# Optimization experiments

Hardware: AMD Instinct MI355X
Metric: run time of the kernel (lower is better)

## Reference

```python
import jax, jax.numpy as jnp
import numpy as np
from jax import lax

DN = ('NCDHW', 'OIDHW', 'NCDHW')


def conv3(x, w, stride=1):
    return lax.conv_general_dilated(x, w, (stride,) * 3, 'VALID', dimension_numbers=DN)


def edge_pad(v):  # zero-gradient (Neumann) halo of width 1
    return jnp.pad(v, ((0, 0), (0, 0), (1, 1), (1, 1), (1, 1)), mode='edge')


def zero_pad(v):  # Dirichlet-0 halo for the MG correction
    return jnp.pad(v, ((0, 0), (0, 0), (1, 1), (1, 1), (1, 1)))


def bc_u(u, ub):  # Neumann everywhere, Dirichlet inlet (u=ub) on -x face
    p = edge_pad(u)
    return p.at[:, :, :, :, 0].set(jnp.asarray(ub, p.dtype))


def prol(x):  # nearest-neighbour upsample x2 (nn.Upsample scale_factor=2)
    for ax in (2, 3, 4):
        x = jnp.repeat(x, 2, axis=ax)
    return x


def setup_inputs() -> dict:
    N = 128
    key = jax.random.key(0)
    k = jax.random.split(key, 6)
    shp = (1, 1, N, N, N)
    # 7-point Laplacian stencil (A and diff)
    wA = np.zeros((1, 1, 3, 3, 3), np.float32)
    wA[0, 0, 1, 1, 1] = -6.0
    for d, h, w in [(0, 1, 1), (2, 1, 1), (1, 0, 1), (1, 2, 1), (1, 1, 0), (1, 1, 2)]:
        wA[0, 0, d, h, w] = 1.0
    w_diff = wA.copy()
    # central-difference advection stencils along W (x), H (y), D (z)
    w_xadv = np.zeros((1, 1, 3, 3, 3), np.float32)
    w_xadv[0, 0, 1, 1, 0], w_xadv[0, 0, 1, 1, 2] = -0.5, 0.5
    w_yadv = np.zeros((1, 1, 3, 3, 3), np.float32)
    w_yadv[0, 0, 1, 0, 1], w_yadv[0, 0, 1, 2, 1] = -0.5, 0.5
    w_zadv = np.zeros((1, 1, 3, 3, 3), np.float32)
    w_zadv[0, 0, 0, 1, 1], w_zadv[0, 0, 2, 1, 1] = -0.5, 0.5
    w_res = np.full((1, 1, 2, 2, 2), 0.125, np.float32)
    return {
        'values_u': jax.random.normal(k[0], shp, jnp.float32) * 0.1,
        'values_v': jax.random.normal(k[1], shp, jnp.float32) * 0.1,
        'values_w': jax.random.normal(k[2], shp, jnp.float32) * 0.1,
        'values_p': jax.random.normal(k[3], shp, jnp.float32) * 0.1,
        'sigma': jax.random.uniform(k[4], shp, jnp.float32) * 10.0,  # solid-body drag field
        'dt': jnp.asarray(0.05, jnp.float32),
        'wA': jnp.asarray(wA), 'w_diff': jnp.asarray(w_diff),
        'w_xadv': jnp.asarray(w_xadv), 'w_yadv': jnp.asarray(w_yadv),
        'w_zadv': jnp.asarray(w_zadv), 'w_res': jnp.asarray(w_res),
        'ub': 1, 'Re': 1, 'iteration': 2, 'nlevel': 9,
    }


def reference(values_u, values_v, values_w, values_p, sigma, dt,
              wA, w_diff, w_xadv, w_yadv, w_zadv, w_res,
              ub, Re, iteration, nlevel):
    diag = wA[0, 0, 1, 1, 1]
    A = lambda x: conv3(x, wA)
    diff = lambda x: conv3(x, w_diff)
    xadv = lambda x: conv3(x, w_xadv)
    yadv = lambda x: conv3(x, w_yadv)
    zadv = lambda x: conv3(x, w_zadv)
    res = lambda x: conv3(x, w_res, stride=2)

    def solid(u, v, w):
        f = 1.0 / (1.0 + dt * sigma)
        return u * f, v * f, w * f

    def pg(uu, vv, ww, u, v, w):  # Petrov-Galerkin dissipation (k fields == 1)
        one = jnp.ones_like(u)
        kp = edge_pad(one)
        ku = 0.5 * (one * diff(uu) + diff(uu * kp) - u * diff(kp))
        kv = 0.5 * (one * diff(vv) + diff(vv * kp) - v * diff(kp))
        kw = 0.5 * (one * diff(ww) + diff(ww * kp) - w * diff(kp))
        return ku, kv, kw

    u, v, w = solid(values_u, values_v, values_w)
    uu, vv, ww = bc_u(u, ub), edge_pad(v), edge_pad(w)
    pp = edge_pad(values_p)
    ku, kv, kw = pg(uu, vv, ww, u, v, w)
    # half-step predictor
    b_u = u + 0.5 * (Re * ku * dt - u * xadv(uu) * dt - v * yadv(uu) * dt - w * zadv(uu) * dt) - xadv(pp) * dt
    b_v = v + 0.5 * (Re * kv * dt - u * xadv(vv) * dt - v * yadv(vv) * dt - w * zadv(vv) * dt) - yadv(pp) * dt
    b_w = w + 0.5 * (Re * kw * dt - u * xadv(ww) * dt - v * yadv(ww) * dt - w * zadv(ww) * dt) - zadv(pp) * dt
    b_u, b_v, b_w = solid(b_u, b_v, b_w)
    buu, bvv, bww = bc_u(b_u, ub), edge_pad(b_v), edge_pad(b_w)
    ku, kv, kw = pg(buu, bvv, bww, b_u, b_v, b_w)
    # full-step corrector
    u = u + Re * ku * dt - b_u * xadv(buu) * dt - b_v * yadv(buu) * dt - b_w * zadv(buu) * dt - xadv(pp) * dt
    v = v + Re * kv * dt - b_u * xadv(bvv) * dt - b_v * yadv(bvv) * dt - b_w * zadv(bvv) * dt - yadv(pp) * dt
    w = w + Re * kw * dt - b_u * xadv(bww) * dt - b_v * yadv(bww) * dt - b_w * zadv(bww) * dt - zadv(pp) * dt
    u, v, w = solid(u, v, w)
    uu, vv, ww = bc_u(u, ub), edge_pad(v), edge_pad(w)
    # multigrid F-cycle pressure solve
    b = -(xadv(uu) + yadv(vv) + zadv(ww)) / dt
    p = values_p
    wmg = jnp.zeros((1, 1, 1, 1, 1), u.dtype)
    r = b
    for _ in range(iteration):
        wmg = jnp.zeros((1, 1, 1, 1, 1), u.dtype)
        r = A(pp) - b
        r_s = [r]
        for _i in range(1, nlevel - 1):
            r = res(r)
            r_s.append(r)
        for i in reversed(range(1, nlevel - 1)):
            wp = zero_pad(wmg)
            wmg = wmg - A(wp) / diag + r_s[i] / diag
            wmg = prol(wmg)
        p = p - wmg
        p = p - A(pp) / diag + b / diag
        pp = edge_pad(p)
    u = u - xadv(pp) * dt
    v = v - yadv(pp) * dt
    w = w - zadv(pp) * dt
    u, v, w = solid(u, v, w)
    return u, v, w, p, wmg, r
```

## Files before the change

### kernel.cpp

```cpp
#include <hip/hip_runtime.h>

#define NN 128
#define VV (NN*NN*NN)

typedef float v4 __attribute__((ext_vector_type(4)));

__device__ __forceinline__ float rcpf(float a){ return __builtin_amdgcn_rcpf(a); }
__device__ __forceinline__ v4 rcp4(v4 a){ v4 r; r.x=rcpf(a.x); r.y=rcpf(a.y); r.z=rcpf(a.z); r.w=rcpf(a.w); return r; }
__device__ __forceinline__ v4 LD4(const float* __restrict__ F, int o){ return *(const v4*)(F+o); }
__device__ __forceinline__ v4 mk4(float a,float b,float c,float d){ v4 r; r.x=a;r.y=b;r.z=c;r.w=d; return r; }

__device__ __forceinline__ int clampi(int a, int lo, int hi){ return min(max(a,lo),hi); }
__device__ __forceinline__ float ldc(const float* __restrict__ f, int z, int y, int x){
    z=clampi(z,0,NN-1); y=clampi(y,0,NN-1); x=clampi(x,0,NN-1);
    return f[(z*NN+y)*NN+x];
}

#define SETUP_OFFS \
    int i4 = (blockIdx.x*blockDim.x + threadIdx.x)<<2; \
    int x = i4 & 127, y = (i4>>7)&127, z = i4>>14; \
    bool x0 = (x==0), x1 = (x==124); \
    int o_c  = i4; \
    int o_ym = o_c + ((y>0)   ? -128   : 0); \
    int o_yp = o_c + ((y<127) ?  128   : 0); \
    int o_zm = o_c + ((z>0)   ? -16384 : 0); \
    int o_zp = o_c + ((z<127) ?  16384 : 0); \
    int o_xm = x0 ? o_c : o_c-1; \
    int o_xp = x1 ? o_c : o_c+4;

__global__ void __launch_bounds__(256) k_predict(
        const float* __restrict__ u_in, const float* __restrict__ v_in,
        const float* __restrict__ w_in, const float* __restrict__ p,
        const float* __restrict__ sg, const float* __restrict__ dtp,
        const int* __restrict__ ubp, const int* __restrict__ rep,
        float* __restrict__ bu, float* __restrict__ bv, float* __restrict__ bw){
    SETUP_OFFS
    float dt = dtp[0], ub = (float)ubp[0], Re = (float)rep[0];
    float h = 0.5f*dt;

    v4 f_c  = rcp4(1.0f + dt*LD4(sg,o_c));
    v4 f_ym = rcp4(1.0f + dt*LD4(sg,o_ym));
    v4 f_yp = rcp4(1.0f + dt*LD4(sg,o_yp));
    v4 f_zm = rcp4(1.0f + dt*LD4(sg,o_zm));
    v4 f_zp = rcp4(1.0f + dt*LD4(sg,o_zp));
    float f_xm = rcpf(1.0f + dt*sg[o_xm]);
    float f_xp = rcpf(1.0f + dt*sg[o_xp]);

#define STEN(F, cen, vxm, vxp, vym, vyp, vzm, vzp, XMVAL) \
    v4 cen = LD4(F,o_c)*f_c; \
    v4 vym = LD4(F,o_ym)*f_ym; v4 vyp = LD4(F,o_yp)*f_yp; \
    v4 vzm = LD4(F,o_zm)*f_zm; v4 vzp = LD4(F,o_zp)*f_zp; \
    float cen##_xms = x0 ? (XMVAL) : F[o_xm]*f_xm; \
    float cen##_xps = x1 ? cen.w   : F[o_xp]*f_xp; \
    v4 vxm = mk4(cen##_xms, cen.x, cen.y, cen.z); \
    v4 vxp = mk4(cen.y, cen.z, cen.w, cen##_xps);

    STEN(u_in, uc, uxm, uxp, uym, uyp, uzm, uzp, ub)
    STEN(v_in, vc, vxm, vxp, vym, vyp, vzm, vzp, vc.x)
    STEN(w_in, wc, wxm, wxp, wym, wyp, wzm, wzp, wc.x)
#undef STEN

    v4 pc = LD4(p,o_c);
    v4 pym = LD4(p,o_ym), pyp = LD4(p,o_yp), pzm = LD4(p,o_zm), pzp = LD4(p,o_zp);
    float p_xms = x0 ? pc.x : p[o_xm];
    float p_xps = x1 ? pc.w : p[o_xp];
    v4 pxm = mk4(p_xms, pc.x, pc.y, pc.z);
    v4 pxp = mk4(pc.y, pc.z, pc.w, p_xps);
    v4 gpx = 0.5f*(pxp-pxm), gpy = 0.5f*(pyp-pym), gpz = 0.5f*(pzp-pzm);

    v4 lap_u = uxm+uxp+uym+uyp+uzm+uzp - 6.0f*uc;
    v4 lap_v = vxm+vxp+vym+vyp+vzm+vzp - 6.0f*vc;
    v4 lap_w = wxm+wxp+wym+wyp+wzm+wzp - 6.0f*wc;
    v4 xau=0.5f*(uxp-uxm), yau=0.5f*(uyp-uym), zau=0.5f*(uzp-uzm);
    v4 xav=0.5f*(vxp-vxm), yav=0.5f*(vyp-vym), zav=0.5f*(vzp-vzm);
    v4 xaw=0.5f*(wxp-wxm), yaw=0.5f*(wyp-wym), zaw=0.5f*(wzp-wzm);

    *(v4*)(bu+o_c) = (uc + h*(Re*lap_u - (uc*xau + vc*yau + wc*zau)) - dt*gpx)*f_c;
    *(v4*)(bv+o_c) = (vc + h*(Re*lap_v - (uc*xav + vc*yav + wc*zav)) - dt*gpy)*f_c;
    *(v4*)(bw+o_c) = (wc + h*(Re*lap_w - (uc*xaw + vc*yaw + wc*zaw)) - dt*gpz)*f_c;
}

__global__ void __launch_bounds__(256) k_corr(
        const float* __restrict__ u_in, const float* __restrict__ v_in,
        const float* __restrict__ w_in,
        const float* __restrict__ bu, const float* __restrict__ bv,
        const float* __restrict__ bw, const float* __restrict__ p,
        const float* __restrict__ sg, const float* __restrict__ dtp,
        const int* __restrict__ ubp, const int* __restrict__ rep,
        float* __restrict__ ou, float* __restrict__ ov, float* __restrict__ ow){
    SETUP_OFFS
    float dt = dtp[0], ub = (float)ubp[0], Re = (float)rep[0];
    v4 f0 = rcp4(1.0f + dt*LD4(sg,o_c));
    v4 u0c = LD4(u_in,o_c)*f0, v0c = LD4(v_in,o_c)*f0, w0c = LD4(w_in,o_c)*f0;

#define STEN2(F, cen, vxm, vxp, vym, vyp, vzm, vzp, XMVAL) \
    v4 cen = LD4(F,o_c); \
    v4 vym = LD4(F,o_ym), vyp = LD4(F,o_yp), vzm = LD4(F,o_zm), vzp = LD4(F,o_zp); \
    float cen##_xms = x0 ? (XMVAL) : F[o_xm]; \
    float cen##_xps = x1 ? cen.w   : F[o_xp]; \
    v4 vxm = mk4(cen##_xms, cen.x, cen.y, cen.z); \
    v4 vxp = mk4(cen.y, cen.z, cen.w, cen##_xps);

    STEN2(bu, uc, uxm, uxp, uym, uyp, uzm, uzp, ub)
    STEN2(bv, vc, vxm, vxp, vym, vyp, vzm, vzp, vc.x)
    STEN2(bw, wc, wxm, wxp, wym, wyp, wzm, wzp, wc.x)

    v4 pc = LD4(p,o_c);
    v4 pym = LD4(p,o_ym), pyp = LD4(p,o_yp), pzm = LD4(p,o_zm), pzp = LD4(p,o_zp);
    float p_xms = x0 ? pc.x : p[o_xm];
    float p_xps = x1 ? pc.w : p[o_xp];
    v4 pxm = mk4(p_xms, pc.x, pc.y, pc.z);
    v4 pxp = mk4(pc.y, pc.z, pc.w, p_xps);
    v4 gpx = 0.5f*(pxp-pxm), gpy = 0.5f*(pyp-pym), gpz = 0.5f*(pzp-pzm);

    v4 lap_u = uxm+uxp+uym+uyp+uzm+uzp - 6.0f*uc;
    v4 lap_v = vxm+vxp+vym+vyp+vzm+vzp - 6.0f*vc;
    v4 lap_w = wxm+wxp+wym+wyp+wzm+wzp - 6.0f*wc;
    v4 xau=0.5f*(uxp-uxm), yau=0.5f*(uyp-uym), zau=0.5f*(uzp-uzm);
    v4 xav=0.5f*(vxp-vxm), yav=0.5f*(vyp-vym), zav=0.5f*(vzp-vzm);
    v4 xaw=0.5f*(wxp-wxm), yaw=0.5f*(wyp-wym), zaw=0.5f*(wzp-wzm);

    *(v4*)(ou+o_c) = (u0c + dt*(Re*lap_u - (uc*xau + vc*yau + wc*zau)) - dt*gpx)*f0;
    *(v4*)(ov+o_c) = (v0c + dt*(Re*lap_v - (uc*xav + vc*yav + wc*zav)) - dt*gpy)*f0;
    *(v4*)(ow+o_c) = (w0c + dt*(Re*lap_w - (uc*xaw + vc*yaw + wc*zaw)) - dt*gpz)*f0;
}

__global__ void __launch_bounds__(256) k_div(
        const float* __restrict__ u, const float* __restrict__ v,
        const float* __restrict__ w, const float* __restrict__ dtp,
        const int* __restrict__ ubp, float* __restrict__ b){
    SETUP_OFFS
    float dt = dtp[0], ub = (float)ubp[0];
    v4 ucv = LD4(u,o_c);
    float u_xms = x0 ? ub    : u[o_xm];
    float u_xps = x1 ? ucv.w : u[o_xp];
    v4 uxm = mk4(u_xms, ucv.x, ucv.y, ucv.z);
    v4 uxp = mk4(ucv.y, ucv.z, ucv.w, u_xps);
    v4 vym = LD4(v,o_ym), vyp = LD4(v,o_yp);
    v4 wzm = LD4(w,o_zm), wzp = LD4(w,o_zp);
    v4 div = 0.5f*((uxp-uxm)+(vyp-vym)+(wzp-wzm));
    *(v4*)(b+o_c) = -div*rcpf(dt);
}

__global__ void k_rr(const float* __restrict__ p, const float* __restrict__ b, float* __restrict__ r1){
    int i = blockIdx.x*blockDim.x + threadIdx.x;
    if (i >= 64*64*64) return;
    int X = i & 63, Y = (i>>6)&63, Z = i>>12;
    float acc = 0.f;
    #pragma unroll
    for (int dz=0;dz<2;++dz)
      #pragma unroll
      for (int dy=0;dy<2;++dy)
        #pragma unroll
        for (int dx=0;dx<2;++dx){
            int z=2*Z+dz, y=2*Y+dy, x=2*X+dx;
            float pc = p[(z*128+y)*128+x];
            float lap = ldc(p,z,y,x-1)+ldc(p,z,y,x+1)+ldc(p,z,y-1,x)+ldc(p,z,y+1,x)
                      + ldc(p,z-1,y,x)+ldc(p,z+1,y,x) - 6.0f*pc;
            acc += lap - b[(z*128+y)*128+x];
        }
    r1[i] = 0.125f*acc;
}

__global__ void k_r2(const float* __restrict__ r1, float* __restrict__ r2){
    int c = blockIdx.x*blockDim.x + threadIdx.x;
    if (c >= 32*32*32) return;
    int X = c & 31, Y = (c>>5)&31, Z = c>>10;
    float a = 0.f;
    #pragma unroll
    for (int dz=0;dz<2;++dz)
      #pragma unroll
      for (int dy=0;dy<2;++dy)
        #pragma unroll
        for (int dx=0;dx<2;++dx)
            a += r1[((2*Z+dz)*64 + (2*Y+dy))*64 + (2*X+dx)];
    r2[c] = 0.125f*a;
}

__device__ void chain_restrict(const float* __restrict__ src, float* __restrict__ dst,
                               int nd, int t, int nt){
    int nd3 = nd*nd*nd, ns = nd*2;
    for (int c = t; c < nd3; c += nt){
        int X = c % nd, Y = (c/nd) % nd, Z = c/(nd*nd);
        float a = 0.f;
        for (int dz=0;dz<2;++dz)
          for (int dy=0;dy<2;++dy)
            for (int dx=0;dx<2;++dx)
                a += src[((2*Z+dz)*ns + (2*Y+dy))*ns + (2*X+dx)];
        dst[c] = 0.125f*a;
    }
}
__device__ void chain_jacobi(const float* __restrict__ jin, const float* __restrict__ r,
                             float* __restrict__ jout, int n, int t, int nt){
    int n3 = n*n*n, hn = n>>1;
    for (int c = t; c < n3; c += nt){
        int X = c % n, Y = (c/n) % n, Z = c/(n*n);
        float s = 0.f;
        s += (X>0  ) ? jin[((Z>>1)*hn+(Y>>1))*hn+((X-1)>>1)] : 0.f;
        s += (X<n-1) ? jin[((Z>>1)*hn+(Y>>1))*hn+((X+1)>>1)] : 0.f;
        s += (Y>0  ) ? jin[((Z>>1)*hn+((Y-1)>>1))*hn+(X>>1)] : 0.f;
        s += (Y<n-1) ? jin[((Z>>1)*hn+((Y+1)>>1))*hn+(X>>1)] : 0.f;
        s += (Z>0  ) ? jin[(((Z-1)>>1)*hn+(Y>>1))*hn+(X>>1)] : 0.f;
        s += (Z<n-1) ? jin[(((Z+1)>>1)*hn+(Y>>1))*hn+(X>>1)] : 0.f;
        jout[c] = (s - r[c]) * (1.0f/6.0f);
    }
}

__global__ void __launch_bounds__(1024) k_chain(const float* __restrict__ r2,
                                                float* __restrict__ j3g, float* __restrict__ r7g){
    __shared__ float r3[4096], r4[512], r5[64], r6[8];
    __shared__ float j7[1], j6[8], j5[64], j4[512], j3[4096];
    int t = threadIdx.x; const int nt = 1024;
    chain_restrict(r2, r3, 16, t, nt); __syncthreads();
    chain_restrict(r3, r4,  8, t, nt); __syncthreads();
    chain_restrict(r4, r5,  4, t, nt); __syncthreads();
    chain_restrict(r5, r6,  2, t, nt); __syncthreads();
    if (t == 0){
        float a = 0.f;
        for (int k=0;k<8;++k) a += r6[k];
        float r7 = 0.125f*a;
        r7g[0] = r7;
        j7[0] = -r7*(1.0f/6.0f);
    }
    __syncthreads();
    chain_jacobi(j7, r6, j6,  2, t, nt); __syncthreads();
    chain_jacobi(j6, r5, j5,  4, t, nt); __syncthreads();
    chain_jacobi(j5, r4, j4,  8, t, nt); __syncthreads();
    chain_jacobi(j4, r3, j3, 16, t, nt); __syncthreads();
    for (int c = t; c < 4096; c += nt) j3g[c] = j3[c];
}

__global__ void k_j2(const float* __restrict__ j3, const float* __restrict__ r2,
                     float* __restrict__ j2){
    int c = blockIdx.x*blockDim.x + threadIdx.x;
    if (c >= 32*32*32) return;
    int X = c & 31, Y = (c>>5)&31, Z = c>>10;
    float s = 0.f;
    s += (X>0 ) ? j3[((Z>>1)*16+(Y>>1))*16+((X-1)>>1)] : 0.f;
    s += (X<31) ? j3[((Z>>1)*16+(Y>>1))*16+((X+1)>>1)] : 0.f;
    s += (Y>0 ) ? j3[((Z>>1)*16+((Y-1)>>1))*16+(X>>1)] : 0.f;
    s += (Y<31) ? j3[((Z>>1)*16+((Y+1)>>1))*16+(X>>1)] : 0.f;
    s += (Z>0 ) ? j3[(((Z-1)>>1)*16+(Y>>1))*16+(X>>1)] : 0.f;
    s += (Z<31) ? j3[(((Z+1)>>1)*16+(Y>>1))*16+(X>>1)] : 0.f;
    j2[c] = (s - r2[c]) * (1.0f/6.0f);
}

__device__ __forceinline__ float j1_eval(const float* __restrict__ r1, const float* __restrict__ j2,
                                         int X, int Y, int Z){
    float s = 0.f;
    s += (X>0 ) ? j2[((Z>>1)*32+(Y>>1))*32+((X-1)>>1)] : 0.f;
    s += (X<63) ? j2[((Z>>1)*32+(Y>>1))*32+((X+1)>>1)] : 0.f;
    s += (Y>0 ) ? j2[((Z>>1)*32+((Y-1)>>1))*32+(X>>1)] : 0.f;
    s += (Y<63) ? j2[((Z>>1)*32+((Y+1)>>1))*32+(X>>1)] : 0.f;
    s += (Z>0 ) ? j2[(((Z-1)>>1)*32+(Y>>1))*32+(X>>1)] : 0.f;
    s += (Z<63) ? j2[(((Z+1)>>1)*32+(Y>>1))*32+(X>>1)] : 0.f;
    return (s - r1[(Z*64+Y)*64+X]) * (1.0f/6.0f);
}

__global__ void __launch_bounds__(256) k_pupd(
        const float* __restrict__ p, const float* __restrict__ r1,
        const float* __restrict__ j2, const float* __restrict__ b,
        float* __restrict__ pout){
    SETUP_OFFS
    v4 pc = LD4(p,o_c);
    v4 pym = LD4(p,o_ym), pyp = LD4(p,o_yp), pzm = LD4(p,o_zm), pzp = LD4(p,o_zp);
    float p_xms = x0 ? pc.x : p[o_xm];
    float p_xps = x1 ? pc.w : p[o_xp];
    v4 pxm = mk4(p_xms, pc.x, pc.y, pc.z);
    v4 pxp = mk4(pc.y, pc.z, pc.w, p_xps);
    v4 lap = pxm+pxp+pym+pyp+pzm+pzp - 6.0f*pc;
    v4 b4 = LD4(b,o_c);
    float j1a = j1_eval(r1, j2, (x>>1),   y>>1, z>>1);
    float j1b = j1_eval(r1, j2, (x>>1)+1, y>>1, z>>1);
    v4 j1v = mk4(j1a, j1a, j1b, j1b);
    *(v4*)(pout+o_c) = pc - j1v + (lap - b4)*(1.0f/6.0f);
}

__global__ void __launch_bounds__(256) k_final(
        const float* __restrict__ u, const float* __restrict__ v,
        const float* __restrict__ w, const float* __restrict__ p,
        const float* __restrict__ r1, const float* __restrict__ j2,
        const float* __restrict__ r7, const float* __restrict__ sg,
        const float* __restrict__ dtp, float* __restrict__ out){
    SETUP_OFFS
    float dt = dtp[0];
    v4 pc = LD4(p,o_c);
    v4 pym = LD4(p,o_ym), pyp = LD4(p,o_yp), pzm = LD4(p,o_zm), pzp = LD4(p,o_zp);
    float p_xms = x0 ? pc.x : p[o_xm];
    float p_xps = x1 ? pc.w : p[o_xp];
    v4 pxm = mk4(p_xms, pc.x, pc.y, pc.z);
    v4 pxp = mk4(pc.y, pc.z, pc.w, p_xps);
    v4 gpx = 0.5f*(pxp-pxm), gpy = 0.5f*(pyp-pym), gpz = 0.5f*(pzp-pzm);
    v4 f0 = rcp4(1.0f + dt*LD4(sg,o_c));
    *(v4*)(out + o_c)              = (LD4(u,o_c) - dt*gpx)*f0;
    *(v4*)(out + (size_t)VV + o_c) = (LD4(v,o_c) - dt*gpy)*f0;
    *(v4*)(out + 2*(size_t)VV + o_c) = (LD4(w,o_c) - dt*gpz)*f0;
    *(v4*)(out + 3*(size_t)VV + o_c) = pc;
    float j1a = j1_eval(r1, j2, (x>>1),   y>>1, z>>1);
    float j1b = j1_eval(r1, j2, (x>>1)+1, y>>1, z>>1);
    *(v4*)(out + 4*(size_t)VV + o_c) = mk4(j1a, j1a, j1b, j1b);
    if (i4 == 0) out[5*(size_t)VV] = r7[0];
}

extern "C" void kernel_launch(void* const* d_in, const int* in_sizes, int n_in,
                              void* d_out, int out_size, void* d_ws, size_t ws_size,
                              hipStream_t stream){
    (void)in_sizes; (void)n_in; (void)out_size; (void)ws_size;
    const float* u_in = (const float*)d_in[0];
    const float* v_in = (const float*)d_in[1];
    const float* w_in = (const float*)d_in[2];
    const float* p_in = (const float*)d_in[3];
    const float* sg   = (const float*)d_in[4];
    const float* dtp  = (const float*)d_in[5];
    const int*  ubp   = (const int*)d_in[12];
    const int*  rep   = (const int*)d_in[13];

    float* ws = (float*)d_ws;
    const size_t V = VV;
    float* bu = ws;
    float* bv = ws +   V;
    float* bw = ws + 2*V;
    float* u  = ws + 3*V;
    float* v  = ws + 4*V;
    float* w  = ws + 5*V;
    float* b  = ws + 6*V;
    float* P1 = ws + 7*V;
    float* P2 = ws + 8*V;
    float* r1 = ws + 9*V;
    float* r2 = r1 + 64*64*64;
    float* j2 = r2 + 32*32*32;
    float* j3 = j2 + 32*32*32;
    float* r7 = j3 + 16*16*16;

    dim3 blk(256);
    int g4 = (VV/4)/256;

    k_predict<<<g4, blk, 0, stream>>>(u_in,v_in,w_in,p_in,sg,dtp,ubp,rep,bu,bv,bw);
    k_corr   <<<g4, blk, 0, stream>>>(u_in,v_in,w_in,bu,bv,bw,p_in,sg,dtp,ubp,rep,u,v,w);
    k_div    <<<g4, blk, 0, stream>>>(u,v,w,dtp,ubp,b);

    const float* pc = p_in;
    float* pn = P1;
    for (int it = 0; it < 2; ++it){
        k_rr   <<<(64*64*64)/256, blk, 0, stream>>>(pc, b, r1);
        k_r2   <<<(32*32*32)/256, blk, 0, stream>>>(r1, r2);
        k_chain<<<1, 1024, 0, stream>>>(r2, j3, r7);
        k_j2   <<<(32*32*32)/256, blk, 0, stream>>>(j3, r2, j2);
        k_pupd <<<g4, blk, 0, stream>>>(pc, r1, j2, b, pn);
        pc = pn; pn = P2;
    }
    k_final<<<g4, blk, 0, stream>>>(u,v,w,pc,r1,j2,r7,sg,dtp,(float*)d_out);
}
```

Measured before the change: 215.8 us.

## Store full-resolution intermediate fields in bf16 to halve workspace traffic

All full-grid intermediates (predicted velocities, corrected velocities, divergence rhs, pressure iterates) are stored in the workspace as bf16 with round-to-nearest-even and widened to fp32 on load. The kernels are memory-bound stencils, so halving the bytes for these buffers cuts DRAM traffic. The multigrid loop is unrolled into explicit float and bf16 template instantiations. The cost is reduced precision in the stored velocity and pressure fields, which may exceed the output tolerance.

```diff
diff --git a/kernel.cpp b/kernel.cpp
--- a/kernel.cpp
+++ b/kernel.cpp
@@ -4,16 +4,38 @@
 #define VV (NN*NN*NN)
 
 typedef float v4 __attribute__((ext_vector_type(4)));
+typedef unsigned short u16;
 
 __device__ __forceinline__ float rcpf(float a){ return __builtin_amdgcn_rcpf(a); }
 __device__ __forceinline__ v4 rcp4(v4 a){ v4 r; r.x=rcpf(a.x); r.y=rcpf(a.y); r.z=rcpf(a.z); r.w=rcpf(a.w); return r; }
-__device__ __forceinline__ v4 LD4(const float* __restrict__ F, int o){ return *(const v4*)(F+o); }
 __device__ __forceinline__ v4 mk4(float a,float b,float c,float d){ v4 r; r.x=a;r.y=b;r.z=c;r.w=d; return r; }
-
 __device__ __forceinline__ int clampi(int a, int lo, int hi){ return min(max(a,lo),hi); }
-__device__ __forceinline__ float ldc(const float* __restrict__ f, int z, int y, int x){
+
+__device__ __forceinline__ float b2f(u16 h){
+    union{unsigned u; float f;} c; c.u = ((unsigned)h)<<16; return c.f;
+}
+__device__ __forceinline__ u16 f2b(float f){
+    union{float f; unsigned u;} c; c.f = f;
+    unsigned u = c.u;
+    unsigned rb = ((u>>16)&1u) + 0x7FFFu;
+    return (u16)((u + rb)>>16);
+}
+__device__ __forceinline__ float ld1(const float* __restrict__ p, int o){ return p[o]; }
+__device__ __forceinline__ float ld1(const u16*  __restrict__ p, int o){ return b2f(p[o]); }
+__device__ __forceinline__ v4 ld4(const float* __restrict__ p, int o){ return *(const v4*)(p+o); }
+__device__ __forceinline__ v4 ld4(const u16*  __restrict__ p, int o){
+    ushort4 h = *(const ushort4*)(p+o);
+    return mk4(b2f(h.x),b2f(h.y),b2f(h.z),b2f(h.w));
+}
+__device__ __forceinline__ void st4(float* __restrict__ p, int o, v4 v){ *(v4*)(p+o) = v; }
+__device__ __forceinline__ void st4(u16*  __restrict__ p, int o, v4 v){
+    ushort4 h; h.x=f2b(v.x); h.y=f2b(v.y); h.z=f2b(v.z); h.w=f2b(v.w);
+    *(ushort4*)(p+o) = h;
+}
+template<typename T>
+__device__ __forceinline__ float ldcT(const T* __restrict__ f, int z, int y, int x){
     z=clampi(z,0,NN-1); y=clampi(y,0,NN-1); x=clampi(x,0,NN-1);
-    return f[(z*NN+y)*NN+x];
+    return ld1(f,(z*NN+y)*NN+x);
 }
 
 #define SETUP_OFFS \
@@ -33,23 +55,23 @@
         const float* __restrict__ w_in, const float* __restrict__ p,
         const float* __restrict__ sg, const float* __restrict__ dtp,
         const int* __restrict__ ubp, const int* __restrict__ rep,
-        float* __restrict__ bu, float* __restrict__ bv, float* __restrict__ bw){
+        u16* __restrict__ bu, u16* __restrict__ bv, u16* __restrict__ bw){
     SETUP_OFFS
     float dt = dtp[0], ub = (float)ubp[0], Re = (float)rep[0];
     float h = 0.5f*dt;
 
-    v4 f_c  = rcp4(1.0f + dt*LD4(sg,o_c));
-    v4 f_ym = rcp4(1.0f + dt*LD4(sg,o_ym));
-    v4 f_yp = rcp4(1.0f + dt*LD4(sg,o_yp));
-    v4 f_zm = rcp4(1.0f + dt*LD4(sg,o_zm));
-    v4 f_zp = rcp4(1.0f + dt*LD4(sg,o_zp));
+    v4 f_c  = rcp4(1.0f + dt*ld4(sg,o_c));
+    v4 f_ym = rcp4(1.0f + dt*ld4(sg,o_ym));
+    v4 f_yp = rcp4(1.0f + dt*ld4(sg,o_yp));
+    v4 f_zm = rcp4(1.0f + dt*ld4(sg,o_zm));
+    v4 f_zp = rcp4(1.0f + dt*ld4(sg,o_zp));
     float f_xm = rcpf(1.0f + dt*sg[o_xm]);
     float f_xp = rcpf(1.0f + dt*sg[o_xp]);
 
 #define STEN(F, cen, vxm, vxp, vym, vyp, vzm, vzp, XMVAL) \
-    v4 cen = LD4(F,o_c)*f_c; \
-    v4 vym = LD4(F,o_ym)*f_ym; v4 vyp = LD4(F,o_yp)*f_yp; \
-    v4 vzm = LD4(F,o_zm)*f_zm; v4 vzp = LD4(F,o_zp)*f_zp; \
+    v4 cen = ld4(F,o_c)*f_c; \
+    v4 vym = ld4(F,o_ym)*f_ym; v4 vyp = ld4(F,o_yp)*f_yp; \
+    v4 vzm = ld4(F,o_zm)*f_zm; v4 vzp = ld4(F,o_zp)*f_zp; \
     float cen##_xms = x0 ? (XMVAL) : F[o_xm]*f_xm; \
     float cen##_xps = x1 ? cen.w   : F[o_xp]*f_xp; \
     v4 vxm = mk4(cen##_xms, cen.x, cen.y, cen.z); \
@@ -60,8 +82,8 @@
     STEN(w_in, wc, wxm, wxp, wym, wyp, wzm, wzp, wc.x)
 #undef STEN
 
-    v4 pc = LD4(p,o_c);
-    v4 pym = LD4(p,o_ym), pyp = LD4(p,o_yp), pzm = LD4(p,o_zm), pzp = LD4(p,o_zp);
+    v4 pc = ld4(p,o_c);
+    v4 pym = ld4(p,o_ym), pyp = ld4(p,o_yp), pzm = ld4(p,o_zm), pzp = ld4(p,o_zp);
     float p_xms = x0 ? pc.x : p[o_xm];
     float p_xps = x1 ? pc.w : p[o_xp];
     v4 pxm = mk4(p_xms, pc.x, pc.y, pc.z);
@@ -75,29 +97,29 @@
     v4 xav=0.5f*(vxp-vxm), yav=0.5f*(vyp-vym), zav=0.5f*(vzp-vzm);
     v4 xaw=0.5f*(wxp-wxm), yaw=0.5f*(wyp-wym), zaw=0.5f*(wzp-wzm);
 
-    *(v4*)(bu+o_c) = (uc + h*(Re*lap_u - (uc*xau + vc*yau + wc*zau)) - dt*gpx)*f_c;
-    *(v4*)(bv+o_c) = (vc + h*(Re*lap_v - (uc*xav + vc*yav + wc*zav)) - dt*gpy)*f_c;
-    *(v4*)(bw+o_c) = (wc + h*(Re*lap_w - (uc*xaw + vc*yaw + wc*zaw)) - dt*gpz)*f_c;
+    st4(bu,o_c, (uc + h*(Re*lap_u - (uc*xau + vc*yau + wc*zau)) - dt*gpx)*f_c);
+    st4(bv,o_c, (vc + h*(Re*lap_v - (uc*xav + vc*yav + wc*zav)) - dt*gpy)*f_c);
+    st4(bw,o_c, (wc + h*(Re*lap_w - (uc*xaw + vc*yaw + wc*zaw)) - dt*gpz)*f_c);
 }
 
 __global__ void __launch_bounds__(256) k_corr(
         const float* __restrict__ u_in, const float* __restrict__ v_in,
         const float* __restrict__ w_in,
-        const float* __restrict__ bu, const float* __restrict__ bv,
-        const float* __restrict__ bw, const float* __restrict__ p,
+        const u16* __restrict__ bu, const u16* __restrict__ bv,
+        const u16* __restrict__ bw, const float* __restrict__ p,
         const float* __restrict__ sg, const float* __restrict__ dtp,
         const int* __restrict__ ubp, const int* __restrict__ rep,
-        float* __restrict__ ou, float* __restrict__ ov, float* __restrict__ ow){
+        u16* __restrict__ ou, u16* __restrict__ ov, u16* __restrict__ ow){
     SETUP_OFFS
     float dt = dtp[0], ub = (float)ubp[0], Re = (float)rep[0];
-    v4 f0 = rcp4(1.0f + dt*LD4(sg,o_c));
-    v4 u0c = LD4(u_in,o_c)*f0, v0c = LD4(v_in,o_c)*f0, w0c = LD4(w_in,o_c)*f0;
+    v4 f0 = rcp4(1.0f + dt*ld4(sg,o_c));
+    v4 u0c = ld4(u_in,o_c)*f0, v0c = ld4(v_in,o_c)*f0, w0c = ld4(w_in,o_c)*f0;
 
 #define STEN2(F, cen, vxm, vxp, vym, vyp, vzm, vzp, XMVAL) \
-    v4 cen = LD4(F,o_c); \
-    v4 vym = LD4(F,o_ym), vyp = LD4(F,o_yp), vzm = LD4(F,o_zm), vzp = LD4(F,o_zp); \
-    float cen##_xms = x0 ? (XMVAL) : F[o_xm]; \
-    float cen##_xps = x1 ? cen.w   : F[o_xp]; \
+    v4 cen = ld4(F,o_c); \
+    v4 vym = ld4(F,o_ym), vyp = ld4(F,o_yp), vzm = ld4(F,o_zm), vzp = ld4(F,o_zp); \
+    float cen##_xms = x0 ? (XMVAL) : ld1(F,o_xm); \
+    float cen##_xps = x1 ? cen.w   : ld1(F,o_xp); \
     v4 vxm = mk4(cen##_xms, cen.x, cen.y, cen.z); \
     v4 vxp = mk4(cen.y, cen.z, cen.w, cen##_xps);
 
@@ -105,8 +127,8 @@
     STEN2(bv, vc, vxm, vxp, vym, vyp, vzm, vzp, vc.x)
     STEN2(bw, wc, wxm, wxp, wym, wyp, wzm, wzp, wc.x)
 
-    v4 pc = LD4(p,o_c);
-    v4 pym = LD4(p,o_ym), pyp = LD4(p,o_yp), pzm = LD4(p,o_zm), pzp = LD4(p,o_zp);
+    v4 pc = ld4(p,o_c);
+    v4 pym = ld4(p,o_ym), pyp = ld4(p,o_yp), pzm = ld4(p,o_zm), pzp = ld4(p,o_zp);
     float p_xms = x0 ? pc.x : p[o_xm];
     float p_xps = x1 ? pc.w : p[o_xp];
     v4 pxm = mk4(p_xms, pc.x, pc.y, pc.z);
@@ -120,29 +142,30 @@
     v4 xav=0.5f*(vxp-vxm), yav=0.5f*(vyp-vym), zav=0.5f*(vzp-vzm);
     v4 xaw=0.5f*(wxp-wxm), yaw=0.5f*(wyp-wym), zaw=0.5f*(wzp-wzm);
 
-    *(v4*)(ou+o_c) = (u0c + dt*(Re*lap_u - (uc*xau + vc*yau + wc*zau)) - dt*gpx)*f0;
-    *(v4*)(ov+o_c) = (v0c + dt*(Re*lap_v - (uc*xav + vc*yav + wc*zav)) - dt*gpy)*f0;
-    *(v4*)(ow+o_c) = (w0c + dt*(Re*lap_w - (uc*xaw + vc*yaw + wc*zaw)) - dt*gpz)*f0;
+    st4(ou,o_c, (u0c + dt*(Re*lap_u - (uc*xau + vc*yau + wc*zau)) - dt*gpx)*f0);
+    st4(ov,o_c, (v0c + dt*(Re*lap_v - (uc*xav + vc*yav + wc*zav)) - dt*gpy)*f0);
+    st4(ow,o_c, (w0c + dt*(Re*lap_w - (uc*xaw + vc*yaw + wc*zaw)) - dt*gpz)*f0);
 }
 
 __global__ void __launch_bounds__(256) k_div(
-        const float* __restrict__ u, const float* __restrict__ v,
-        const float* __restrict__ w, const float* __restrict__ dtp,
-        const int* __restrict__ ubp, float* __restrict__ b){
+        const u16* __restrict__ u, const u16* __restrict__ v,
+        const u16* __restrict__ w, const float* __restrict__ dtp,
+        const int* __restrict__ ubp, u16* __restrict__ b){
     SETUP_OFFS
     float dt = dtp[0], ub = (float)ubp[0];
-    v4 ucv = LD4(u,o_c);
-    float u_xms = x0 ? ub    : u[o_xm];
-    float u_xps = x1 ? ucv.w : u[o_xp];
+    v4 ucv = ld4(u,o_c);
+    float u_xms = x0 ? ub    : ld1(u,o_xm);
+    float u_xps = x1 ? ucv.w : ld1(u,o_xp);
     v4 uxm = mk4(u_xms, ucv.x, ucv.y, ucv.z);
     v4 uxp = mk4(ucv.y, ucv.z, ucv.w, u_xps);
-    v4 vym = LD4(v,o_ym), vyp = LD4(v,o_yp);
-    v4 wzm = LD4(w,o_zm), wzp = LD4(w,o_zp);
+    v4 vym = ld4(v,o_ym), vyp = ld4(v,o_yp);
+    v4 wzm = ld4(w,o_zm), wzp = ld4(w,o_zp);
     v4 div = 0.5f*((uxp-uxm)+(vyp-vym)+(wzp-wzm));
-    *(v4*)(b+o_c) = -div*rcpf(dt);
-}
-
-__global__ void k_rr(const float* __restrict__ p, const float* __restrict__ b, float* __restrict__ r1){
+    st4(b,o_c, -div*rcpf(dt));
+}
+
+template<typename PT>
+__global__ void k_rr(const PT* __restrict__ p, const u16* __restrict__ b, float* __restrict__ r1){
     int i = blockIdx.x*blockDim.x + threadIdx.x;
     if (i >= 64*64*64) return;
     int X = i & 63, Y = (i>>6)&63, Z = i>>12;
@@ -154,10 +177,10 @@
         #pragma unroll
         for (int dx=0;dx<2;++dx){
             int z=2*Z+dz, y=2*Y+dy, x=2*X+dx;
-            float pc = p[(z*128+y)*128+x];
-            float lap = ldc(p,z,y,x-1)+ldc(p,z,y,x+1)+ldc(p,z,y-1,x)+ldc(p,z,y+1,x)
-                      + ldc(p,z-1,y,x)+ldc(p,z+1,y,x) - 6.0f*pc;
-            acc += lap - b[(z*128+y)*128+x];
+            float pc = ld1(p,(z*128+y)*128+x);
+            float lap = ldcT(p,z,y,x-1)+ldcT(p,z,y,x+1)+ldcT(p,z,y-1,x)+ldcT(p,z,y+1,x)
+                      + ldcT(p,z-1,y,x)+ldcT(p,z+1,y,x) - 6.0f*pc;
+            acc += lap - ld1(b,(z*128+y)*128+x);
         }
     r1[i] = 0.125f*acc;
 }
@@ -257,48 +280,49 @@
     return (s - r1[(Z*64+Y)*64+X]) * (1.0f/6.0f);
 }
 
+template<typename PT>
 __global__ void __launch_bounds__(256) k_pupd(
-        const float* __restrict__ p, const float* __restrict__ r1,
-        const float* __restrict__ j2, const float* __restrict__ b,
-        float* __restrict__ pout){
-    SETUP_OFFS
-    v4 pc = LD4(p,o_c);
-    v4 pym = LD4(p,o_ym), pyp = LD4(p,o_yp), pzm = LD4(p,o_zm), pzp = LD4(p,o_zp);
-    float p_xms = x0 ? pc.x : p[o_xm];
-    float p_xps = x1 ? pc.w : p[o_xp];
+        const PT* __restrict__ p, const float* __restrict__ r1,
+        const float* __restrict__ j2, const u16* __restrict__ b,
+        u16* __restrict__ pout){
+    SETUP_OFFS
+    v4 pc = ld4(p,o_c);
+    v4 pym = ld4(p,o_ym), pyp = ld4(p,o_yp), pzm = ld4(p,o_zm), pzp = ld4(p,o_zp);
+    float p_xms = x0 ? pc.x : ld1(p,o_xm);
+    float p_xps = x1 ? pc.w : ld1(p,o_xp);
     v4 pxm = mk4(p_xms, pc.x, pc.y, pc.z);
     v4 pxp = mk4(pc.y, pc.z, pc.w, p_xps);
     v4 lap = pxm+pxp+pym+pyp+pzm+pzp - 6.0f*pc;
-    v4 b4 = LD4(b,o_c);
+    v4 b4 = ld4(b,o_c);
     float j1a = j1_eval(r1, j2, (x>>1),   y>>1, z>>1);
     float j1b = j1_eval(r1, j2, (x>>1)+1, y>>1, z>>1);
     v4 j1v = mk4(j1a, j1a, j1b, j1b);
-    *(v4*)(pout+o_c) = pc - j1v + (lap - b4)*(1.0f/6.0f);
+    st4(pout,o_c, pc - j1v + (lap - b4)*(1.0f/6.0f));
 }
 
 __global__ void __launch_bounds__(256) k_final(
-        const float* __restrict__ u, const float* __restrict__ v,
-        const float* __restrict__ w, const float* __restrict__ p,
+        const u16* __restrict__ u, const u16* __restrict__ v,
+        const u16* __restrict__ w, const u16* __restrict__ p,
         const float* __restrict__ r1, const float* __restrict__ j2,
         const float* __restrict__ r7, const float* __restrict__ sg,
         const float* __restrict__ dtp, float* __restrict__ out){
     SETUP_OFFS
     float dt = dtp[0];
-    v4 pc = LD4(p,o_c);
-    v4 pym = LD4(p,o_ym), pyp = LD4(p,o_yp), pzm = LD4(p,o_zm), pzp = LD4(p,o_zp);
-    float p_xms = x0 ? pc.x : p[o_xm];
-    float p_xps = x1 ? pc.w : p[o_xp];
+    v4 pc = ld4(p,o_c);
+    v4 pym = ld4(p,o_ym), pyp = ld4(p,o_yp), pzm = ld4(p,o_zm), pzp = ld4(p,o_zp);
+    float p_xms = x0 ? pc.x : ld1(p,o_xm);
+    float p_xps = x1 ? pc.w : ld1(p,o_xp);
     v4 pxm = mk4(p_xms, pc.x, pc.y, pc.z);
     v4 pxp = mk4(pc.y, pc.z, pc.w, p_xps);
     v4 gpx = 0.5f*(pxp-pxm), gpy = 0.5f*(pyp-pym), gpz = 0.5f*(pzp-pzm);
-    v4 f0 = rcp4(1.0f + dt*LD4(sg,o_c));
-    *(v4*)(out + o_c)              = (LD4(u,o_c) - dt*gpx)*f0;
-    *(v4*)(out + (size_t)VV + o_c) = (LD4(v,o_c) - dt*gpy)*f0;
-    *(v4*)(out + 2*(size_t)VV + o_c) = (LD4(w,o_c) - dt*gpz)*f0;
-    *(v4*)(out + 3*(size_t)VV + o_c) = pc;
+    v4 f0 = rcp4(1.0f + dt*ld4(sg,o_c));
+    st4(out, o_c,                        (ld4(u,o_c) - dt*gpx)*f0);
+    st4(out + (size_t)VV, o_c,           (ld4(v,o_c) - dt*gpy)*f0);
+    st4(out + 2*(size_t)VV, o_c,         (ld4(w,o_c) - dt*gpz)*f0);
+    st4(out + 3*(size_t)VV, o_c,         pc);
     float j1a = j1_eval(r1, j2, (x>>1),   y>>1, z>>1);
     float j1b = j1_eval(r1, j2, (x>>1)+1, y>>1, z>>1);
-    *(v4*)(out + 4*(size_t)VV + o_c) = mk4(j1a, j1a, j1b, j1b);
+    st4(out + 4*(size_t)VV, o_c,         mk4(j1a, j1a, j1b, j1b));
     if (i4 == 0) out[5*(size_t)VV] = r7[0];
 }
 
@@ -315,18 +339,19 @@
     const int*  ubp   = (const int*)d_in[12];
     const int*  rep   = (const int*)d_in[13];
 
-    float* ws = (float*)d_ws;
+    u16* wh = (u16*)d_ws;
     const size_t V = VV;
-    float* bu = ws;
-    float* bv = ws +   V;
-    float* bw = ws + 2*V;
-    float* u  = ws + 3*V;
-    float* v  = ws + 4*V;
-    float* w  = ws + 5*V;
-    float* b  = ws + 6*V;
-    float* P1 = ws + 7*V;
-    float* P2 = ws + 8*V;
-    float* r1 = ws + 9*V;
+    u16* bu = wh;
+    u16* bv = wh +   V;
+    u16* bw = wh + 2*V;
+    u16* u  = wh + 3*V;
+    u16* v  = wh + 4*V;
+    u16* w  = wh + 5*V;
+    u16* b  = wh + 6*V;
+    u16* P1 = wh + 7*V;
+    u16* P2 = wh + 8*V;
+    float* fs = (float*)(wh + 10*V);
+    float* r1 = fs;
     float* r2 = r1 + 64*64*64;
     float* j2 = r2 + 32*32*32;
     float* j3 = j2 + 32*32*32;
@@ -339,15 +364,17 @@
     k_corr   <<<g4, blk, 0, stream>>>(u_in,v_in,w_in,bu,bv,bw,p_in,sg,dtp,ubp,rep,u,v,w);
     k_div    <<<g4, blk, 0, stream>>>(u,v,w,dtp,ubp,b);
 
-    const float* pc = p_in;
-    float* pn = P1;
-    for (int it = 0; it < 2; ++it){
-        k_rr   <<<(64*64*64)/256, blk, 0, stream>>>(pc, b, r1);
-        k_r2   <<<(32*32*32)/256, blk, 0, stream>>>(r1, r2);
-        k_chain<<<1, 1024, 0, stream>>>(r2, j3, r7);
-        k_j2   <<<(32*32*32)/256, blk, 0, stream>>>(j3, r2, j2);
-        k_pupd <<<g4, blk, 0, stream>>>(pc, r1, j2, b, pn);
-        pc = pn; pn = P2;
-    }
-    k_final<<<g4, blk, 0, stream>>>(u,v,w,pc,r1,j2,r7,sg,dtp,(float*)d_out);
-}
+    k_rr<float><<<(64*64*64)/256, blk, 0, stream>>>(p_in, b, r1);
+    k_r2        <<<(32*32*32)/256, blk, 0, stream>>>(r1, r2);
+    k_chain     <<<1, 1024, 0, stream>>>(r2, j3, r7);
+    k_j2        <<<(32*32*32)/256, blk, 0, stream>>>(j3, r2, j2);
+    k_pupd<float><<<g4, blk, 0, stream>>>(p_in, r1, j2, b, P1);
+
+    k_rr<u16>  <<<(64*64*64)/256, blk, 0, stream>>>(P1, b, r1);
+    k_r2       <<<(32*32*32)/256, blk, 0, stream>>>(r1, r2);
+    k_chain    <<<1, 1024, 0, stream>>>(r2, j3, r7);
+    k_j2       <<<(32*32*32)/256, blk, 0, stream>>>(j3, r2, j2);
+    k_pupd<u16><<<g4, blk, 0, stream>>>(P1, r1, j2, b, P2);
+
+    k_final<<<g4, blk, 0, stream>>>(u,v,w,P2,r1,j2,r7,sg,dtp,(float*)d_out);
+}
```

New measurement: 205.3 us. -4.8%, faster.
